# Optimization experiments

Hardware: AMD Instinct MI355X
Metric: run time of the kernel (lower is better)

## Reference

```python
import jax, jax.numpy as jnp
import numpy as np

B, L, D = 4, 2048, 1024
H, KD, VD = 16, 64, 64
EPS = 1e-5


def setup_inputs() -> dict:
    key = jax.random.key(0)
    ks = jax.random.split(key, 12)
    s_in = 1.0 / np.sqrt(D)
    s_out = 1.0 / np.sqrt(H * VD)
    return {
        "queries": jax.random.normal(ks[0], (B, L, D), dtype=jnp.float32),
        "Wq": jax.random.uniform(ks[1], (D, H * KD), jnp.float32, -s_in, s_in),
        "bq": jax.random.uniform(ks[2], (H * KD,), jnp.float32, -s_in, s_in),
        "Wk": jax.random.uniform(ks[3], (D, H * KD), jnp.float32, -s_in, s_in),
        "bk": jax.random.uniform(ks[4], (H * KD,), jnp.float32, -s_in, s_in),
        "Wv": jax.random.uniform(ks[5], (D, H * VD), jnp.float32, -s_in, s_in),
        "bv": jax.random.uniform(ks[6], (H * VD,), jnp.float32, -s_in, s_in),
        "Wo": jax.random.uniform(ks[7], (H * VD, D), jnp.float32, -s_out, s_out),
        "bo": jax.random.uniform(ks[8], (D,), jnp.float32, -s_out, s_out),
        "gamma": jnp.ones((D,), jnp.float32),
        "beta": jnp.zeros((D,), jnp.float32),
    }


def reference(queries, Wq, bq, Wk, bk, Wv, bv, Wo, bo, gamma, beta):
    # QKV projections -> [B, L, H, head_dim]
    q = (queries @ Wq + bq).reshape(B, L, H, KD)
    k = (queries @ Wk + bk).reshape(B, L, H, KD)
    v = (queries @ Wv + bv).reshape(B, L, H, VD)
    # scaled dot-product attention per head: scores [B, H, Lq, Lk]
    scores = jnp.einsum("bqhd,bkhd->bhqk", q, k) / np.sqrt(KD).astype(np.float32)
    attn = jax.nn.softmax(scores, axis=-1)
    out = jnp.einsum("bhqk,bkhd->bqhd", attn, v).reshape(B, L, H * VD)
    # out projection (dropout is identity in eval), residual + LayerNorm
    res = out @ Wo + bo + queries
    mu = jnp.mean(res, axis=-1, keepdims=True)
    var = jnp.var(res, axis=-1, keepdims=True)
    return (res - mu) / jnp.sqrt(var + EPS) * gamma + beta
```

## Files before the change

### kernel.cpp

```cpp
#include <hip/hip_runtime.h>
#include <hip/hip_bf16.h>

#define BATCH 4
#define SEQ   2048
#define DIM   1024
#define NHEAD 16
#define HDIM  64
#define EPS_LN 1e-5f
#define QSCALE 0.18033688011112042f

typedef __attribute__((ext_vector_type(8))) short short8;
typedef __attribute__((ext_vector_type(4))) float f32x4;
typedef __attribute__((ext_vector_type(16))) float f32x16;
typedef __attribute__((ext_vector_type(4))) unsigned uint32x4;

__device__ __forceinline__ unsigned short f2bf(float x) {
    __hip_bfloat16 h = __float2bfloat16(x);
    return *reinterpret_cast<unsigned short*>(&h);
}
__device__ __forceinline__ unsigned int pack2bf(float a, float b) {
    __hip_bfloat162 h = __float22bfloat162_rn(float2{a, b});
    return *reinterpret_cast<unsigned int*>(&h);
}

__device__ __forceinline__ void pl32_swap(unsigned& a, unsigned& b) {
    asm("v_permlane32_swap_b32 %0, %1" : "+v"(a), "+v"(b));
}

__device__ __forceinline__ void gl_lds16(const void* g, void* l) {
    __builtin_amdgcn_global_load_lds(
        (const __attribute__((address_space(1))) unsigned int*)g,
        (__attribute__((address_space(3))) unsigned int*)l,
        16, 0, 0);
}

__global__ __launch_bounds__(256) void prep_kernel(const float* __restrict__ W0,
                                                   const float* __restrict__ W1,
                                                   const float* __restrict__ W2,
                                                   const float* __restrict__ W3,
                                                   const float* __restrict__ queries,
                                                   unsigned short* __restrict__ Wqkvt,
                                                   unsigned short* __restrict__ Wot,
                                                   unsigned short* __restrict__ qout)
{
    const int z = blockIdx.z;
    const int t = threadIdx.x;

    if (z == 4) {
        const int nthr = 16 * 16 * 256;
        int i = (blockIdx.y * 16 + blockIdx.x) * 256 + t;
        for (int it = 0; it < (BATCH * SEQ * DIM / 4) / nthr; it++, i += nthr) {
            float4 v = ((const float4*)queries)[i];
            ushort4 u;
            u.x = f2bf(v.x); u.y = f2bf(v.y); u.z = f2bf(v.z); u.w = f2bf(v.w);
            ((ushort4*)qout)[i] = u;
        }
        return;
    }

    __shared__ float Ts[64][65];
    const float* W = (z == 0) ? W0 : (z == 1) ? W1 : (z == 2) ? W2 : W3;
    unsigned short* Wt = (z == 3) ? Wot : (Wqkvt + (size_t)z * DIM * DIM);

    const int k0 = blockIdx.y * 64, n0 = blockIdx.x * 64;
    const int lr = t >> 2, lq = t & 3;

#pragma unroll
    for (int i = 0; i < 4; i++) {
        float4 v = *(const float4*)(W + (size_t)(k0 + lr) * DIM + n0 + (lq * 4 + i) * 4);
        Ts[lr][(lq * 4 + i) * 4 + 0] = v.x;
        Ts[lr][(lq * 4 + i) * 4 + 1] = v.y;
        Ts[lr][(lq * 4 + i) * 4 + 2] = v.z;
        Ts[lr][(lq * 4 + i) * 4 + 3] = v.w;
    }
    __syncthreads();
#pragma unroll
    for (int i = 0; i < 4; i++) {
        const int c = lq * 16 + i * 4;
        ushort4 u;
        u.x = f2bf(Ts[c + 0][lr]);
        u.y = f2bf(Ts[c + 1][lr]);
        u.z = f2bf(Ts[c + 2][lr]);
        u.w = f2bf(Ts[c + 3][lr]);
        *(ushort4*)(Wt + (size_t)(n0 + lr) * DIM + k0 + c) = u;
    }
}

__global__ __launch_bounds__(256) void gemm_qkv(const unsigned short* __restrict__ A,
                                                const unsigned short* __restrict__ Bt,
                                                const float* __restrict__ bq,
                                                const float* __restrict__ bk,
                                                const float* __restrict__ bv,
                                                unsigned short* __restrict__ Qbf,
                                                unsigned short* __restrict__ Kbf,
                                                unsigned short* __restrict__ Vtb)
{
    __shared__ __attribute__((aligned(16))) unsigned short As[128 * 32];
    __shared__ __attribute__((aligned(16))) unsigned short Bs[128 * 32];

    const int tid = threadIdx.x;
    const int w = tid >> 6, lane = tid & 63;
    const int col = lane & 15, quad = lane >> 4;
    const int wm = (w >> 1) * 64, wn = (w & 1) * 64;
    const int m0 = blockIdx.y * 128, n0 = blockIdx.x * 128;

    f32x4 acc[4][4] = {};
    const int srow = tid >> 2, sc4 = tid & 3;

    for (int k0 = 0; k0 < DIM; k0 += 32) {
        __syncthreads();
#pragma unroll
        for (int it = 0; it < 2; it++) {
            gl_lds16(A  + (size_t)(m0 + srow + it * 64) * DIM + k0 + sc4 * 8,
                     (char*)As + w * 1024 + it * 4096);
            gl_lds16(Bt + (size_t)(n0 + srow + it * 64) * DIM + k0 + sc4 * 8,
                     (char*)Bs + w * 1024 + it * 4096);
        }
        __syncthreads();

        short8 af[4], bf[4];
#pragma unroll
        for (int mt = 0; mt < 4; mt++) af[mt] = *(short8*)&As[(wm + mt * 16 + col) * 32 + quad * 8];
#pragma unroll
        for (int nt = 0; nt < 4; nt++) bf[nt] = *(short8*)&Bs[(wn + nt * 16 + col) * 32 + quad * 8];

#pragma unroll
        for (int mt = 0; mt < 4; mt++)
#pragma unroll
            for (int nt = 0; nt < 4; nt++)
                acc[mt][nt] = __builtin_amdgcn_mfma_f32_16x16x32_bf16(af[mt], bf[nt], acc[mt][nt], 0, 0, 0);
    }

    const int sector = n0 >> 10;
    const float* bias = (sector == 0) ? bq : (sector == 1) ? bk : bv;

#pragma unroll
    for (int nt = 0; nt < 4; nt++) {
        const int n = n0 + wn + nt * 16 + col;
        const int nloc = n - (sector << 10);
        const float bvv = bias[nloc];
#pragma unroll
        for (int mt = 0; mt < 4; mt++) {
            const int mbase = m0 + wm + mt * 16 + quad * 4;
            if (sector == 0) {
#pragma unroll
                for (int r = 0; r < 4; r++)
                    Qbf[(size_t)(mbase + r) * DIM + nloc] = f2bf((acc[mt][nt][r] + bvv) * QSCALE);
            } else if (sector == 1) {
#pragma unroll
                for (int r = 0; r < 4; r++)
                    Kbf[(size_t)(mbase + r) * DIM + nloc] = f2bf(acc[mt][nt][r] + bvv);
            } else {
                const int h = nloc >> 6, d = nloc & 63;
                const int b = mbase >> 11, l = mbase & 2047;
                ushort4 u;
                u.x = f2bf(acc[mt][nt][0] + bvv);
                u.y = f2bf(acc[mt][nt][1] + bvv);
                u.z = f2bf(acc[mt][nt][2] + bvv);
                u.w = f2bf(acc[mt][nt][3] + bvv);
                *(ushort4*)(Vtb + ((size_t)((b * NHEAD + h) * HDIM + d)) * SEQ + l) = u;
            }
        }
    }
}

__global__ __launch_bounds__(256) void gemm_out(const unsigned short* __restrict__ A,
                                                const unsigned short* __restrict__ Bt,
                                                const float* __restrict__ bias,
                                                const float* __restrict__ resid,
                                                float* __restrict__ Cout)
{
    __shared__ __attribute__((aligned(16))) unsigned short As[128 * 32];
    __shared__ __attribute__((aligned(16))) unsigned short Bs[128 * 32];

    const int tid = threadIdx.x;
    const int w = tid >> 6, lane = tid & 63;
    const int col = lane & 15, quad = lane >> 4;
    const int wm = (w >> 1) * 64, wn = (w & 1) * 64;
    const int m0 = blockIdx.y * 128, n0 = blockIdx.x * 128;

    f32x4 acc[4][4] = {};
    const int srow = tid >> 2, sc4 = tid & 3;

    for (int k0 = 0; k0 < DIM; k0 += 32) {
        __syncthreads();
#pragma unroll
        for (int it = 0; it < 2; it++) {
            gl_lds16(A  + (size_t)(m0 + srow + it * 64) * DIM + k0 + sc4 * 8,
                     (char*)As + w * 1024 + it * 4096);
            gl_lds16(Bt + (size_t)(n0 + srow + it * 64) * DIM + k0 + sc4 * 8,
                     (char*)Bs + w * 1024 + it * 4096);
        }
        __syncthreads();

        short8 af[4], bf[4];
#pragma unroll
        for (int mt = 0; mt < 4; mt++) af[mt] = *(short8*)&As[(wm + mt * 16 + col) * 32 + quad * 8];
#pragma unroll
        for (int nt = 0; nt < 4; nt++) bf[nt] = *(short8*)&Bs[(wn + nt * 16 + col) * 32 + quad * 8];

#pragma unroll
        for (int mt = 0; mt < 4; mt++)
#pragma unroll
            for (int nt = 0; nt < 4; nt++)
                acc[mt][nt] = __builtin_amdgcn_mfma_f32_16x16x32_bf16(af[mt], bf[nt], acc[mt][nt], 0, 0, 0);
    }

#pragma unroll
    for (int nt = 0; nt < 4; nt++) {
        const int n = n0 + wn + nt * 16 + col;
        const float bvv = bias[n];
#pragma unroll
        for (int mt = 0; mt < 4; mt++) {
            const int mbase = m0 + wm + mt * 16 + quad * 4;
#pragma unroll
            for (int r = 0; r < 4; r++) {
                const size_t off = (size_t)(mbase + r) * DIM + n;
                Cout[off] = acc[mt][nt][r] + bvv + resid[off];
            }
        }
    }
}

__global__ __launch_bounds__(256) void attn_mfma(const unsigned short* __restrict__ Qb,
                                                 const unsigned short* __restrict__ Kb,
                                                 const unsigned short* __restrict__ Vt,
                                                 unsigned short* __restrict__ Ob)
{
    __shared__ __attribute__((aligned(16))) unsigned short Ks[2 * 64 * 64];
    __shared__ __attribute__((aligned(16))) unsigned short Vs[2 * 64 * 64];

    const int tid = threadIdx.x;
    const int w = tid >> 6, lane = tid & 63;
    const int l31 = lane & 31, hi = lane >> 5;
    const int sw7 = l31 & 7;

    const int bh  = blockIdx.x & 63;
    const int qt_ = blockIdx.x >> 6;
    const int b   = bh >> 4;
    const int h   = bh & 15;

    const int q0 = qt_ * 128 + w * 32;

    short8 qf[4];
#pragma unroll
    for (int ds = 0; ds < 4; ds++)
        qf[ds] = *(const short8*)(Qb + ((size_t)(b * SEQ) + q0 + l31) * DIM + h * HDIM + ds * 16 + hi * 8);

    f32x16 o[2] = {};
    float dsum = 0.f;

    const size_t kbase0 = ((size_t)(b * SEQ)) * DIM + h * HDIM;
    const size_t vbase0 = ((size_t)((b * NHEAD + h) * HDIM)) * SEQ;

    const int lr  = lane >> 3;
    const int swc = (lane & 7) ^ lr;

#pragma unroll
    for (int i = 0; i < 2; i++) {
        const int row = w * 16 + i * 8 + lr;
        gl_lds16(Kb + kbase0 + (size_t)row * DIM + swc * 8, (char*)Ks + w * 2048 + i * 1024);
        gl_lds16(Vt + vbase0 + (size_t)row * SEQ + swc * 8, (char*)Vs + w * 2048 + i * 1024);
    }
    __syncthreads();

    for (int kt = 0; kt < SEQ / 64; kt++) {
        const int cur = kt & 1, nxt = cur ^ 1;
        const unsigned short* Ksb = Ks + cur * 4096;
        const unsigned short* Vsb = Vs + cur * 4096;

        if (kt + 1 < SEQ / 64) {
#pragma unroll
            for (int i = 0; i < 2; i++) {
                const int row = w * 16 + i * 8 + lr;
                gl_lds16(Kb + kbase0 + (size_t)((kt + 1) * 64 + row) * DIM + swc * 8,
                         (char*)Ks + nxt * 8192 + w * 2048 + i * 1024);
                gl_lds16(Vt + vbase0 + (size_t)row * SEQ + (kt + 1) * 64 + swc * 8,
                         (char*)Vs + nxt * 8192 + w * 2048 + i * 1024);
            }
        }

        short8 pf[2][2];
#pragma unroll
        for (int kb = 0; kb < 2; kb++) {
            f32x16 s = {};
#pragma unroll
            for (int ds = 0; ds < 4; ds++) {
                short8 kf = *(const short8*)&Ksb[(kb * 32 + l31) * 64 + (((ds * 2 + hi) ^ sw7) * 8)];
                s = __builtin_amdgcn_mfma_f32_32x32x16_bf16(kf, qf[ds], s, 0, 0, 0);
            }
            unsigned d0, d1, d2, d3, d4, d5, d6, d7;
            {
                float p0, p1;
                p0 = __builtin_amdgcn_exp2f(s[0]);  p1 = __builtin_amdgcn_exp2f(s[1]);
                dsum += p0 + p1;  d0 = pack2bf(p0, p1);
                p0 = __builtin_amdgcn_exp2f(s[2]);  p1 = __builtin_amdgcn_exp2f(s[3]);
                dsum += p0 + p1;  d1 = pack2bf(p0, p1);
                p0 = __builtin_amdgcn_exp2f(s[4]);  p1 = __builtin_amdgcn_exp2f(s[5]);
                dsum += p0 + p1;  d2 = pack2bf(p0, p1);
                p0 = __builtin_amdgcn_exp2f(s[6]);  p1 = __builtin_amdgcn_exp2f(s[7]);
                dsum += p0 + p1;  d3 = pack2bf(p0, p1);
                p0 = __builtin_amdgcn_exp2f(s[8]);  p1 = __builtin_amdgcn_exp2f(s[9]);
                dsum += p0 + p1;  d4 = pack2bf(p0, p1);
                p0 = __builtin_amdgcn_exp2f(s[10]); p1 = __builtin_amdgcn_exp2f(s[11]);
                dsum += p0 + p1;  d5 = pack2bf(p0, p1);
                p0 = __builtin_amdgcn_exp2f(s[12]); p1 = __builtin_amdgcn_exp2f(s[13]);
                dsum += p0 + p1;  d6 = pack2bf(p0, p1);
                p0 = __builtin_amdgcn_exp2f(s[14]); p1 = __builtin_amdgcn_exp2f(s[15]);
                dsum += p0 + p1;  d7 = pack2bf(p0, p1);
            }
            pl32_swap(d0, d2);  pl32_swap(d1, d3);
            pl32_swap(d4, d6);  pl32_swap(d5, d7);
            pf[kb][0] = __builtin_bit_cast(short8, uint32x4{d0, d1, d2, d3});
            pf[kb][1] = __builtin_bit_cast(short8, uint32x4{d4, d5, d6, d7});
        }

        __builtin_amdgcn_s_setprio(1);
#pragma unroll
        for (int db = 0; db < 2; db++)
#pragma unroll
            for (int kb = 0; kb < 2; kb++)
#pragma unroll
                for (int ks = 0; ks < 2; ks++) {
                    short8 vf = *(const short8*)&Vsb[(db * 32 + l31) * 64 + (((kb * 4 + ks * 2 + hi) ^ sw7) * 8)];
                    o[db] = __builtin_amdgcn_mfma_f32_32x32x16_bf16(vf, pf[kb][ks], o[db], 0, 0, 0);
                }
        __builtin_amdgcn_s_setprio(0);

        __syncthreads();
    }

    const float den = dsum + __shfl_xor(dsum, 32);
    const float inv = 1.f / den;

    const size_t rowoff = ((size_t)(b * SEQ) + q0 + l31) * DIM + h * HDIM;
#pragma unroll
    for (int db = 0; db < 2; db++)
#pragma unroll
        for (int g = 0; g < 4; g++) {
            ushort4 u;
            u.x = f2bf(o[db][g * 4 + 0] * inv);
            u.y = f2bf(o[db][g * 4 + 1] * inv);
            u.z = f2bf(o[db][g * 4 + 2] * inv);
            u.w = f2bf(o[db][g * 4 + 3] * inv);
            *(ushort4*)(Ob + rowoff + db * 32 + g * 8 + hi * 4) = u;
        }
}

__global__ __launch_bounds__(256) void layernorm_kernel(float* __restrict__ res,
                                                        const float* __restrict__ gamma,
                                                        const float* __restrict__ beta)
{
    const int tid = threadIdx.x;
    const int row = blockIdx.x;
    float4 xv = ((const float4*)(res + (size_t)row * DIM))[tid];

    float s  = xv.x + xv.y + xv.z + xv.w;
    float sq = xv.x * xv.x + xv.y * xv.y + xv.z * xv.z + xv.w * xv.w;
#pragma unroll
    for (int off = 32; off; off >>= 1) {
        s  += __shfl_xor(s, off);
        sq += __shfl_xor(sq, off);
    }
    __shared__ float sm[8];
    const int w = tid >> 6, lane = tid & 63;
    if (lane == 0) { sm[w] = s; sm[4 + w] = sq; }
    __syncthreads();
    const float st  = sm[0] + sm[1] + sm[2] + sm[3];
    const float sqt = sm[4] + sm[5] + sm[6] + sm[7];
    const float mu   = st * (1.f / DIM);
    const float var  = sqt * (1.f / DIM) - mu * mu;
    const float rstd = rsqrtf(var + EPS_LN);

    float4 g  = ((const float4*)gamma)[tid];
    float4 be = ((const float4*)beta)[tid];
    float4 o;
    o.x = (xv.x - mu) * rstd * g.x + be.x;
    o.y = (xv.y - mu) * rstd * g.y + be.y;
    o.z = (xv.z - mu) * rstd * g.z + be.z;
    o.w = (xv.w - mu) * rstd * g.w + be.w;
    ((float4*)(res + (size_t)row * DIM))[tid] = o;
}

extern "C" void kernel_launch(void* const* d_in, const int* in_sizes, int n_in,
                              void* d_out, int out_size, void* d_ws, size_t ws_size,
                              hipStream_t stream)
{
    const float* queries = (const float*)d_in[0];
    const float* Wq = (const float*)d_in[1];
    const float* bq = (const float*)d_in[2];
    const float* Wk = (const float*)d_in[3];
    const float* bk = (const float*)d_in[4];
    const float* Wv = (const float*)d_in[5];
    const float* bv = (const float*)d_in[6];
    const float* Wo = (const float*)d_in[7];
    const float* bo = (const float*)d_in[8];
    const float* gamma = (const float*)d_in[9];
    const float* beta  = (const float*)d_in[10];
    float* outp = (float*)d_out;

    const int M = BATCH * SEQ;
    const size_t BUF = (size_t)M * DIM;
    const size_t WSZ = (size_t)DIM * DIM;

    unsigned short* w0  = (unsigned short*)d_ws;
    unsigned short* qin = w0;
    unsigned short* Qbf = w0 + BUF;
    unsigned short* Kbf = w0 + 2 * BUF;
    unsigned short* Vtb = w0 + 3 * BUF;
    unsigned short* Wqkvt = w0 + 4 * BUF;
    unsigned short* Wot   = Wqkvt + 3 * WSZ;
    unsigned short* Obf = qin;

    dim3 blk(256);

    dim3 pgrid(DIM / 64, DIM / 64, 5);
    prep_kernel<<<pgrid, blk, 0, stream>>>(Wq, Wk, Wv, Wo, queries, Wqkvt, Wot, qin);

    dim3 qkvgrid(3 * DIM / 128, M / 128);
    gemm_qkv<<<qkvgrid, blk, 0, stream>>>(qin, Wqkvt, bq, bk, bv, Qbf, Kbf, Vtb);

    attn_mfma<<<BATCH * NHEAD * (SEQ / 128), blk, 0, stream>>>(Qbf, Kbf, Vtb, Obf);

    dim3 ogrid(DIM / 128, M / 128);
    gemm_out<<<ogrid, blk, 0, stream>>>(Obf, Wot, bo, queries, outp);

    layernorm_kernel<<<M, blk, 0, stream>>>(outp, gamma, beta);
}
```

Measured before the change: 318.8 us.

## Split attention key tiles across two wave groups with LDS reduction

The attention kernel now launches 512 threads per block. Two groups of four waves each take one 32-key half of every 64-key tile for the same 128 queries, and each wave does half the QK and PV MFMA work per tile. At the end, the second group writes its partial output and row sums to LDS, reusing the K/V buffers, and the first group combines them and writes the result. This is meant to raise the number of active waves and hide latency, at the cost of an extra LDS reduction step and more pressure on each block-wide barrier.

```diff
diff --git a/kernel.cpp b/kernel.cpp
--- a/kernel.cpp
+++ b/kernel.cpp
@@ -222,16 +222,18 @@
     }
 }
 
-__global__ __launch_bounds__(256) void attn_mfma(const unsigned short* __restrict__ Qb,
+__global__ __launch_bounds__(512) void attn_mfma(const unsigned short* __restrict__ Qb,
                                                  const unsigned short* __restrict__ Kb,
                                                  const unsigned short* __restrict__ Vt,
                                                  unsigned short* __restrict__ Ob)
 {
     __shared__ __attribute__((aligned(16))) unsigned short Ks[2 * 64 * 64];
     __shared__ __attribute__((aligned(16))) unsigned short Vs[2 * 64 * 64];
+    __shared__ float DsX[128];
 
     const int tid = threadIdx.x;
     const int w = tid >> 6, lane = tid & 63;
+    const int qw = w & 3, kw = w >> 2;
     const int l31 = lane & 31, hi = lane >> 5;
     const int sw7 = l31 & 7;
 
@@ -240,7 +242,7 @@
     const int b   = bh >> 4;
     const int h   = bh & 15;
 
-    const int q0 = qt_ * 128 + w * 32;
+    const int q0 = qt_ * 128 + qw * 32;
 
     short8 qf[4];
 #pragma unroll
@@ -256,11 +258,10 @@
     const int lr  = lane >> 3;
     const int swc = (lane & 7) ^ lr;
 
-#pragma unroll
-    for (int i = 0; i < 2; i++) {
-        const int row = w * 16 + i * 8 + lr;
-        gl_lds16(Kb + kbase0 + (size_t)row * DIM + swc * 8, (char*)Ks + w * 2048 + i * 1024);
-        gl_lds16(Vt + vbase0 + (size_t)row * SEQ + swc * 8, (char*)Vs + w * 2048 + i * 1024);
+    {
+        const int row = w * 8 + lr;
+        gl_lds16(Kb + kbase0 + (size_t)row * DIM + swc * 8, (char*)Ks + w * 1024);
+        gl_lds16(Vt + vbase0 + (size_t)row * SEQ + swc * 8, (char*)Vs + w * 1024);
     }
     __syncthreads();
 
@@ -270,81 +271,90 @@
         const unsigned short* Vsb = Vs + cur * 4096;
 
         if (kt + 1 < SEQ / 64) {
-#pragma unroll
-            for (int i = 0; i < 2; i++) {
-                const int row = w * 16 + i * 8 + lr;
-                gl_lds16(Kb + kbase0 + (size_t)((kt + 1) * 64 + row) * DIM + swc * 8,
-                         (char*)Ks + nxt * 8192 + w * 2048 + i * 1024);
-                gl_lds16(Vt + vbase0 + (size_t)row * SEQ + (kt + 1) * 64 + swc * 8,
-                         (char*)Vs + nxt * 8192 + w * 2048 + i * 1024);
+            const int row = w * 8 + lr;
+            gl_lds16(Kb + kbase0 + (size_t)((kt + 1) * 64 + row) * DIM + swc * 8,
+                     (char*)Ks + nxt * 8192 + w * 1024);
+            gl_lds16(Vt + vbase0 + (size_t)row * SEQ + (kt + 1) * 64 + swc * 8,
+                     (char*)Vs + nxt * 8192 + w * 1024);
+        }
+
+        f32x16 s = {};
+#pragma unroll
+        for (int ds = 0; ds < 4; ds++) {
+            short8 kf = *(const short8*)&Ksb[(kw * 32 + l31) * 64 + (((ds * 2 + hi) ^ sw7) * 8)];
+            s = __builtin_amdgcn_mfma_f32_32x32x16_bf16(kf, qf[ds], s, 0, 0, 0);
+        }
+        unsigned d0, d1, d2, d3, d4, d5, d6, d7;
+        {
+            float p0, p1;
+            p0 = __builtin_amdgcn_exp2f(s[0]);  p1 = __builtin_amdgcn_exp2f(s[1]);
+            dsum += p0 + p1;  d0 = pack2bf(p0, p1);
+            p0 = __builtin_amdgcn_exp2f(s[2]);  p1 = __builtin_amdgcn_exp2f(s[3]);
+            dsum += p0 + p1;  d1 = pack2bf(p0, p1);
+            p0 = __builtin_amdgcn_exp2f(s[4]);  p1 = __builtin_amdgcn_exp2f(s[5]);
+            dsum += p0 + p1;  d2 = pack2bf(p0, p1);
+            p0 = __builtin_amdgcn_exp2f(s[6]);  p1 = __builtin_amdgcn_exp2f(s[7]);
+            dsum += p0 + p1;  d3 = pack2bf(p0, p1);
+            p0 = __builtin_amdgcn_exp2f(s[8]);  p1 = __builtin_amdgcn_exp2f(s[9]);
+            dsum += p0 + p1;  d4 = pack2bf(p0, p1);
+            p0 = __builtin_amdgcn_exp2f(s[10]); p1 = __builtin_amdgcn_exp2f(s[11]);
+            dsum += p0 + p1;  d5 = pack2bf(p0, p1);
+            p0 = __builtin_amdgcn_exp2f(s[12]); p1 = __builtin_amdgcn_exp2f(s[13]);
+            dsum += p0 + p1;  d6 = pack2bf(p0, p1);
+            p0 = __builtin_amdgcn_exp2f(s[14]); p1 = __builtin_amdgcn_exp2f(s[15]);
+            dsum += p0 + p1;  d7 = pack2bf(p0, p1);
+        }
+        pl32_swap(d0, d2);  pl32_swap(d1, d3);
+        pl32_swap(d4, d6);  pl32_swap(d5, d7);
+        short8 pf0 = __builtin_bit_cast(short8, uint32x4{d0, d1, d2, d3});
+        short8 pf1 = __builtin_bit_cast(short8, uint32x4{d4, d5, d6, d7});
+
+        __builtin_amdgcn_s_setprio(1);
+#pragma unroll
+        for (int db = 0; db < 2; db++) {
+            short8 vf0 = *(const short8*)&Vsb[(db * 32 + l31) * 64 + (((kw * 4 + 0 + hi) ^ sw7) * 8)];
+            short8 vf1 = *(const short8*)&Vsb[(db * 32 + l31) * 64 + (((kw * 4 + 2 + hi) ^ sw7) * 8)];
+            o[db] = __builtin_amdgcn_mfma_f32_32x32x16_bf16(vf0, pf0, o[db], 0, 0, 0);
+            o[db] = __builtin_amdgcn_mfma_f32_32x32x16_bf16(vf1, pf1, o[db], 0, 0, 0);
+        }
+        __builtin_amdgcn_s_setprio(0);
+
+        __syncthreads();
+    }
+
+    const float ds_h = dsum + __shfl_xor(dsum, 32);
+
+    if (kw == 1) {
+        if (hi == 0) DsX[qw * 32 + l31] = ds_h;
+        float* p0 = (float*)Ks + (size_t)(qw * 64 + lane) * 16;
+        float* p1 = (float*)Vs + (size_t)(qw * 64 + lane) * 16;
+        *(f32x16*)p0 = o[0];
+        *(f32x16*)p1 = o[1];
+    }
+    __syncthreads();
+    if (kw == 0) {
+        const float den = ds_h + DsX[qw * 32 + l31];
+        const float inv = 1.f / den;
+        const float* p0 = (const float*)Ks + (size_t)(qw * 64 + lane) * 16;
+        const float* p1 = (const float*)Vs + (size_t)(qw * 64 + lane) * 16;
+        const f32x16 o0p = *(const f32x16*)p0;
+        const f32x16 o1p = *(const f32x16*)p1;
+        o[0] += o0p;
+        o[1] += o1p;
+
+        const size_t rowoff = ((size_t)(b * SEQ) + q0 + l31) * DIM + h * HDIM;
+#pragma unroll
+        for (int db = 0; db < 2; db++)
+#pragma unroll
+            for (int g = 0; g < 4; g++) {
+                ushort4 u;
+                u.x = f2bf(o[db][g * 4 + 0] * inv);
+                u.y = f2bf(o[db][g * 4 + 1] * inv);
+                u.z = f2bf(o[db][g * 4 + 2] * inv);
+                u.w = f2bf(o[db][g * 4 + 3] * inv);
+                *(ushort4*)(Ob + rowoff + db * 32 + g * 8 + hi * 4) = u;
             }
-        }
-
-        short8 pf[2][2];
-#pragma unroll
-        for (int kb = 0; kb < 2; kb++) {
-            f32x16 s = {};
-#pragma unroll
-            for (int ds = 0; ds < 4; ds++) {
-                short8 kf = *(const short8*)&Ksb[(kb * 32 + l31) * 64 + (((ds * 2 + hi) ^ sw7) * 8)];
-                s = __builtin_amdgcn_mfma_f32_32x32x16_bf16(kf, qf[ds], s, 0, 0, 0);
-            }
-            unsigned d0, d1, d2, d3, d4, d5, d6, d7;
-            {
-                float p0, p1;
-                p0 = __builtin_amdgcn_exp2f(s[0]);  p1 = __builtin_amdgcn_exp2f(s[1]);
-                dsum += p0 + p1;  d0 = pack2bf(p0, p1);
-                p0 = __builtin_amdgcn_exp2f(s[2]);  p1 = __builtin_amdgcn_exp2f(s[3]);
-                dsum += p0 + p1;  d1 = pack2bf(p0, p1);
-                p0 = __builtin_amdgcn_exp2f(s[4]);  p1 = __builtin_amdgcn_exp2f(s[5]);
-                dsum += p0 + p1;  d2 = pack2bf(p0, p1);
-                p0 = __builtin_amdgcn_exp2f(s[6]);  p1 = __builtin_amdgcn_exp2f(s[7]);
-                dsum += p0 + p1;  d3 = pack2bf(p0, p1);
-                p0 = __builtin_amdgcn_exp2f(s[8]);  p1 = __builtin_amdgcn_exp2f(s[9]);
-                dsum += p0 + p1;  d4 = pack2bf(p0, p1);
-                p0 = __builtin_amdgcn_exp2f(s[10]); p1 = __builtin_amdgcn_exp2f(s[11]);
-                dsum += p0 + p1;  d5 = pack2bf(p0, p1);
-                p0 = __builtin_amdgcn_exp2f(s[12]); p1 = __builtin_amdgcn_exp2f(s[13]);
-                dsum += p0 + p1;  d6 = pack2bf(p0, p1);
-                p0 = __builtin_amdgcn_exp2f(s[14]); p1 = __builtin_amdgcn_exp2f(s[15]);
-                dsum += p0 + p1;  d7 = pack2bf(p0, p1);
-            }
-            pl32_swap(d0, d2);  pl32_swap(d1, d3);
-            pl32_swap(d4, d6);  pl32_swap(d5, d7);
-            pf[kb][0] = __builtin_bit_cast(short8, uint32x4{d0, d1, d2, d3});
-            pf[kb][1] = __builtin_bit_cast(short8, uint32x4{d4, d5, d6, d7});
-        }
-
-        __builtin_amdgcn_s_setprio(1);
-#pragma unroll
-        for (int db = 0; db < 2; db++)
-#pragma unroll
-            for (int kb = 0; kb < 2; kb++)
-#pragma unroll
-                for (int ks = 0; ks < 2; ks++) {
-                    short8 vf = *(const short8*)&Vsb[(db * 32 + l31) * 64 + (((kb * 4 + ks * 2 + hi) ^ sw7) * 8)];
-                    o[db] = __builtin_amdgcn_mfma_f32_32x32x16_bf16(vf, pf[kb][ks], o[db], 0, 0, 0);
-                }
-        __builtin_amdgcn_s_setprio(0);
-
-        __syncthreads();
-    }
-
-    const float den = dsum + __shfl_xor(dsum, 32);
-    const float inv = 1.f / den;
-
-    const size_t rowoff = ((size_t)(b * SEQ) + q0 + l31) * DIM + h * HDIM;
-#pragma unroll
-    for (int db = 0; db < 2; db++)
-#pragma unroll
-        for (int g = 0; g < 4; g++) {
-            ushort4 u;
-            u.x = f2bf(o[db][g * 4 + 0] * inv);
-            u.y = f2bf(o[db][g * 4 + 1] * inv);
-            u.z = f2bf(o[db][g * 4 + 2] * inv);
-            u.w = f2bf(o[db][g * 4 + 3] * inv);
-            *(ushort4*)(Ob + rowoff + db * 32 + g * 8 + hi * 4) = u;
-        }
+    }
 }
 
 __global__ __launch_bounds__(256) void layernorm_kernel(float* __restrict__ res,
@@ -420,7 +430,7 @@
     dim3 qkvgrid(3 * DIM / 128, M / 128);
     gemm_qkv<<<qkvgrid, blk, 0, stream>>>(qin, Wqkvt, bq, bk, bv, Qbf, Kbf, Vtb);
 
-    attn_mfma<<<BATCH * NHEAD * (SEQ / 128), blk, 0, stream>>>(Qbf, Kbf, Vtb, Obf);
+    attn_mfma<<<BATCH * NHEAD * (SEQ / 128), dim3(512), 0, stream>>>(Qbf, Kbf, Vtb, Obf);
 
     dim3 ogrid(DIM / 128, M / 128);
     gemm_out<<<ogrid, blk, 0, stream>>>(Obf, Wot, bo, queries, outp);
```

Result: faster. 311.6 us (-2.2%).
